# Optimization experiments

Measured on AMD Instinct MI355X. Metric: run time of the kernel, lower is better.

## Reference

```python
import jax, jax.numpy as jnp
import numpy as np

# Graph layout: B equal-sized graphs, contiguous node ids.
B, NG, EG = 64, 2000, 64000          # graphs, nodes/graph, edges/graph
K = 1600                              # ceil(0.8 * NG) — TopKPooling ratio=0.8
N, E = B * NG, B * EG
FEAT_DIM, EMB, G1, G2, DENSE, NCLS = 10000, 64, 32, 32, 64, 10


def setup_inputs() -> dict:
    key = jax.random.key(0)
    ks = jax.random.split(key, 12)
    x = jax.random.randint(ks[0], (N, 1), 0, FEAT_DIM)
    # random edges within each graph, then offset by graph base node id
    e = jax.random.randint(ks[1], (2, B, EG), 0, NG) + (jnp.arange(B) * NG)[None, :, None]
    edge_index = e.reshape(2, E)
    batch = jnp.repeat(jnp.arange(B), NG)
    sc = 0.05
    return {
        "x": x, "edge_index": edge_index, "batch": batch,
        "emb": jax.random.normal(ks[2], (FEAT_DIM, EMB), jnp.float32) * sc,
        "W1": jax.random.normal(ks[3], (EMB, G1), jnp.float32) * sc,
        "b1": jnp.zeros((G1,), jnp.float32),
        "W2": jax.random.normal(ks[4], (G1, G2), jnp.float32) * sc,
        "b2": jnp.zeros((G2,), jnp.float32),
        "pool_w": jax.random.normal(ks[5], (G2,), jnp.float32) * sc,
        "dense_W": jax.random.normal(ks[6], (G2, DENSE), jnp.float32) * sc,
        "dense_b": jnp.zeros((DENSE,), jnp.float32),
        "out_W": jax.random.normal(ks[7], (DENSE, NCLS), jnp.float32) * sc,
        "out_b": jnp.zeros((NCLS,), jnp.float32),
    }


def gcn_layer(h, src, dst, W, b):
    """PyG GCNConv: add self-loops, symmetric D^-1/2 A D^-1/2 aggregation."""
    n = h.shape[0]
    loop = jnp.arange(n)
    s = jnp.concatenate([src, loop])
    d = jnp.concatenate([dst, loop])
    h = h @ W                                                   # [N, out]
    deg = jax.ops.segment_sum(jnp.ones_like(d, dtype=h.dtype), d, num_segments=n)
    dinv = jnp.where(deg > 0, deg ** -0.5, 0.0)
    norm = dinv[s] * dinv[d]                                    # [E+N]
    out = jax.ops.segment_sum(h[s] * norm[:, None], d, num_segments=n)
    return out + b


def reference(x, edge_index, batch, emb, W1, b1, W2, b2, pool_w,
              dense_W, dense_b, out_W, out_b):
    h = emb[x[:, 0]]                                            # [N, EMB]
    src, dst = edge_index[0], edge_index[1]
    h = jax.nn.relu(gcn_layer(h, src, dst, W1, b1))
    h = jax.nn.relu(gcn_layer(h, src, dst, W2, b2))
    # TopKPooling: score = tanh(x.w / ||w||); keep top ceil(0.8*NG) per graph,
    # scale kept features by their scores. Equal graph sizes -> static shapes.
    score = jnp.tanh(h @ pool_w / jnp.linalg.norm(pool_w))      # [N]
    sb = score.reshape(B, NG)
    hb = h.reshape(B, NG, G2)
    vals, idx = jax.lax.top_k(sb, K)                            # [B, K]
    hp = jnp.take_along_axis(hb, idx[:, :, None], axis=1) * vals[:, :, None]
    g = hp.max(axis=1)                                          # global max pool [B, G2]
    d = jax.nn.relu(g @ dense_W + dense_b)
    return d @ out_W + out_b                                    # [B, NCLS]
```

## Files before the change

### kernel.cpp

```cpp
#include <hip/hip_runtime.h>
#include <hip/hip_fp16.h>
#include <math.h>

#define NB 64
#define NGRAPH 2000
#define EGRAPH 64000
#define NN (NB*NGRAPH)
#define NE (NB*EGRAPH)
#define KSEL 1600
#define FEAT 10000
#define EMBD 64
#define G1D 32
#define G2D 32
#define DENSED 64
#define NCLSD 10
#define NCHUNK 8
#define CHUNK_E (EGRAPH/NCHUNK)
#define NQD 8
#define QNODES (NGRAPH/NQD)
#define LOUT_CAP 10000
#define AGG_PARTS 4
#define NPP (NGRAPH/AGG_PARTS)


__device__ __forceinline__ float4 ld_row8h(const char* base, unsigned byteoff)
{
    uint2 u = *(const uint2*)(base + byteoff);
    __half2 p0 = *(__half2*)&u.x;
    __half2 p1 = *(__half2*)&u.y;
    float2 f0 = __half22float2(p0);
    float2 f1 = __half22float2(p1);
    return make_float4(f0.x, f0.y, f1.x, f1.y);
}

__device__ __forceinline__ void st_row8h(__half* dst, float4 v)
{
    __half2 p0 = __floats2half2_rn(v.x, v.y);
    __half2 p1 = __floats2half2_rn(v.z, v.w);
    uint2 u;
    u.x = *(unsigned*)&p0;
    u.y = *(unsigned*)&p1;
    *(uint2*)dst = u;
}

__device__ __forceinline__ void acc8h(const char* base, unsigned off,
                                      __half2& lo, __half2& hi)
{
    uint2 u = *(const uint2*)(base + off);
    lo = __hadd2(lo, *(__half2*)&u.x);
    hi = __hadd2(hi, *(__half2*)&u.y);
}

__device__ __forceinline__ float4 h2tof4(__half2 lo, __half2 hi)
{
    float2 a = __half22float2(lo);
    float2 b = __half22float2(hi);
    return make_float4(a.x, a.y, b.x, b.y);
}

__global__ __launch_bounds__(256) void prep_kernel(const int* __restrict__ ei,
                                                   int* __restrict__ chist,
                                                   const float* __restrict__ emb,
                                                   const float* __restrict__ W1,
                                                   float* __restrict__ embW)
{
    __shared__ float shmem[2048];
    const int tid = threadIdx.x;
    if (blockIdx.x < 512) {
        int* hist = (int*)shmem;
        const int lb = blockIdx.x;
        const int xcd = lb & 7, t = lb >> 3;
        const int g = xcd * 8 + (t >> 3);
        const int q = t & 7;
        const int base_e = g * EGRAPH + q * CHUNK_E;
        const int base_n = g * NGRAPH;
        for (int v = tid; v < NGRAPH; v += 256) hist[v] = 0;
        __syncthreads();
        for (int k = tid; k < CHUNK_E; k += 256) {
            int d = ei[NE + base_e + k];
            atomicAdd(&hist[d - base_n], 1);
        }
        __syncthreads();
        int* out = chist + (size_t)(g * NCHUNK + q) * NGRAPH;
        for (int v = tid; v < NGRAPH; v += 256) out[v] = hist[v];
    } else {
        float* W1s = shmem;
        for (int i = tid; i < EMBD * G1D; i += 256) W1s[i] = W1[i];
        __syncthreads();
        int id = (blockIdx.x - 512) * 256 + tid;
        int r = id >> 5, c = id & 31;
        if (r >= FEAT) return;
        const float* er = emb + r * EMBD;
        float acc = 0.f;
        #pragma unroll 8
        for (int k = 0; k < EMBD; ++k) acc += er[k] * W1s[k * G1D + c];
        embW[r * G1D + c] = acc;
    }
}

__global__ __launch_bounds__(256) void scan_graph(const int* __restrict__ chist,
                                                  float* __restrict__ dinv,
                                                  int* __restrict__ row_start)
{
    __shared__ int hist[NGRAPH];
    __shared__ int csA[256];
    __shared__ int csB[256];
    const int b = (blockIdx.x & 7) * 8 + (blockIdx.x >> 3);
    const int tid = threadIdx.x;
    const int base_n = b * NGRAPH, base_e = b * EGRAPH;
    const int* ch = chist + (size_t)b * NCHUNK * NGRAPH;

    for (int v = tid; v < NGRAPH; v += 256) {
        int tot = 0;
        #pragma unroll
        for (int q = 0; q < NCHUNK; ++q) tot += ch[q * NGRAPH + v];
        hist[v] = tot;
        dinv[base_n + v] = rsqrtf((float)(tot + 1));
    }
    __syncthreads();
    if (tid < 250) {
        int s = 0;
        #pragma unroll
        for (int i = 0; i < 8; ++i) s += hist[tid * 8 + i];
        csA[tid] = s;
    }
    __syncthreads();
    int* sb = csA; int* db = csB;
    for (int off = 1; off < 256; off <<= 1) {
        int v = 0;
        if (tid < 250) { v = sb[tid]; if (tid >= off) v += sb[tid - off]; }
        if (tid < 250) db[tid] = v;
        __syncthreads();
        int* t = sb; sb = db; db = t;
    }
    if (tid < 250) {
        int run = (tid == 0) ? 0 : sb[tid - 1];
        #pragma unroll
        for (int i = 0; i < 8; ++i) {
            int idx = tid * 8 + i;
            int c = hist[idx];
            row_start[base_n + idx] = base_e + run;
            run += c;
        }
    }
}

__global__ __launch_bounds__(1024) void mid_kernel(const int* __restrict__ ei,
                                                   const int* __restrict__ row_start,
                                                   int* __restrict__ csr,
                                                   const int* __restrict__ x,
                                                   const float* __restrict__ embW,
                                                   const float* __restrict__ dinv,
                                                   __half* __restrict__ A)
{
    __shared__ int cur[QNODES];
    __shared__ int lout[LOUT_CAP];
    const int tid = threadIdx.x;
    if (blockIdx.x < 512) {
        const int lb = blockIdx.x;
        const int xcd = lb & 7, t = lb >> 3;
        const int g = xcd * 8 + (t >> 3);
        const int qd = t & 7;
        const int base_n = g * NGRAPH;
        const int lo = qd * QNODES;
        const int base = row_start[base_n + lo];
        const int qend = (g == NB - 1 && qd == NQD - 1) ? NE
                         : row_start[base_n + lo + QNODES];
        for (int v = tid; v < QNODES; v += 1024)
            cur[v] = row_start[base_n + lo + v] - base;
        __syncthreads();
        const int4* srcp = (const int4*)(ei + g * EGRAPH);
        const int4* dstp = (const int4*)(ei + NE + g * EGRAPH);
        const int sub = base_n + lo;
        for (int k = tid; k < EGRAPH / 4; k += 1024) {
            int4 d4 = dstp[k];
            int4 s4 = srcp[k];
            int d, pos, sl;
            d = d4.x - sub;
            if ((unsigned)d < (unsigned)QNODES) {
                pos = atomicAdd(&cur[d], 1);
                sl = s4.x - base_n;
                if (pos < LOUT_CAP) lout[pos] = (sl << 6) + (sl << 3);
            }
            d = d4.y - sub;
            if ((unsigned)d < (unsigned)QNODES) {
                pos = atomicAdd(&cur[d], 1);
                sl = s4.y - base_n;
                if (pos < LOUT_CAP) lout[pos] = (sl << 6) + (sl << 3);
            }
            d = d4.z - sub;
            if ((unsigned)d < (unsigned)QNODES) {
                pos = atomicAdd(&cur[d], 1);
                sl = s4.z - base_n;
                if (pos < LOUT_CAP) lout[pos] = (sl << 6) + (sl << 3);
            }
            d = d4.w - sub;
            if ((unsigned)d < (unsigned)QNODES) {
                pos = atomicAdd(&cur[d], 1);
                sl = s4.w - base_n;
                if (pos < LOUT_CAP) lout[pos] = (sl << 6) + (sl << 3);
            }
        }
        __syncthreads();
        int size = qend - base;
        if (size > LOUT_CAP) size = LOUT_CAP;
        for (int i = tid; i < size; i += 1024)
            csr[base + i] = lout[i];
    } else {
        int id = (blockIdx.x - 512) * 1024 + tid;
        int v = id >> 3, r = id & 7;
        int xv = x[v];
        float dv = dinv[v];
        float4 e = ((const float4*)(embW + (size_t)xv * G1D))[r];
        e.x *= dv; e.y *= dv; e.z *= dv; e.w *= dv;
        st_row8h(A + (size_t)v * G1D + r * 4, e);
    }
}


__global__ __launch_bounds__(1024) void agg1_kernel(const __half* __restrict__ Ain,
                                                    const float* __restrict__ dinv,
                                                    const int* __restrict__ row_start,
                                                    const int* __restrict__ csr,
                                                    const float* __restrict__ b1,
                                                    const float* __restrict__ W2,
                                                    __half* __restrict__ Bout)
{
    __shared__ uint2 table2[NGRAPH * 9];
    __shared__ float hsh[32][G2D];
    const int lb = blockIdx.x;
    const int xcd = lb & 7, t = lb >> 3;
    const int b = xcd * 8 + (t >> 2);
    const int part = t & 3;
    const int tid = threadIdx.x;
    const int base_n = b * NGRAPH;

    {
        const uint2* src = (const uint2*)(Ain + (size_t)base_n * G1D);
        for (int i = tid; i < NGRAPH * 8; i += 1024)
            table2[(i >> 3) * 9 + (i & 7)] = src[i];
    }
    __syncthreads();

    const char* Lbase = (const char*)table2;
    const int hw = tid >> 5;
    const int hl = tid & 31;
    const int slot = hl >> 3;
    const int r = hl & 7;
    const int roff = r << 3;
    const float4 bias4 = ((const float4*)b1)[r];

    float w2c[G1D];
    #pragma unroll
    for (int k = 0; k < G1D; ++k) w2c[k] = W2[k * G2D + hl];

    const __half2 z2 = __float2half2_rn(0.f);

    const int vloc0 = part * NPP + hw * 16;
    const int vend = part * NPP + NPP;
    int v = base_n + vloc0;
    int rs = row_start[v];
    int re = (v == NN - 1) ? NE : row_start[v + 1];
    int s0 = csr[rs + slot];
    int s1 = csr[rs + slot + 4];
    int s2 = csr[rs + slot + 8];
    int s3 = csr[rs + slot + 12];

    for (int i = 0; i < 16; ++i) {
        int vloc = vloc0 + i;
        if (vloc >= vend) break;
        int re_next = (v + 1 >= NN - 1) ? NE : row_start[v + 2];
        int n0 = csr[re + slot];
        int n1 = csr[re + slot + 4];
        int n2 = csr[re + slot + 8];
        int n3 = csr[re + slot + 12];

        int me = rs + ((re - rs) & ~15);
        __half2 l0 = z2, h0 = z2, l1 = z2, h1 = z2;
        __half2 l2 = z2, h2 = z2, l3 = z2, h3 = z2;
        if (slot == 0)
            acc8h(Lbase, (unsigned)((vloc << 6) + (vloc << 3) + roff), l0, h0);
        int j = rs + slot;
        while (j < me) {
            int jn = j + 16;
            int t0 = csr[jn];
            int t1 = csr[jn + 4];
            int t2 = csr[jn + 8];
            int t3 = csr[jn + 12];
            acc8h(Lbase, (unsigned)(s0 + roff), l0, h0);
            acc8h(Lbase, (unsigned)(s1 + roff), l1, h1);
            acc8h(Lbase, (unsigned)(s2 + roff), l2, h2);
            acc8h(Lbase, (unsigned)(s3 + roff), l3, h3);
            j = jn; s0 = t0; s1 = t1; s2 = t2; s3 = t3;
        }
        {
            int jt = me + slot;
            if (jt < re)      acc8h(Lbase, (unsigned)(s0 + roff), l0, h0);
            if (jt + 4 < re)  acc8h(Lbase, (unsigned)(s1 + roff), l1, h1);
            if (jt + 8 < re)  acc8h(Lbase, (unsigned)(s2 + roff), l2, h2);
            if (jt + 12 < re) acc8h(Lbase, (unsigned)(s3 + roff), l3, h3);
        }
        float4 f0 = h2tof4(l0, h0);
        float4 f1 = h2tof4(l1, h1);
        float4 f2 = h2tof4(l2, h2);
        float4 f3 = h2tof4(l3, h3);
        float4 acc;
        acc.x = (f0.x + f1.x) + (f2.x + f3.x);
        acc.y = (f0.y + f1.y) + (f2.y + f3.y);
        acc.z = (f0.z + f1.z) + (f2.z + f3.z);
        acc.w = (f0.w + f1.w) + (f2.w + f3.w);
        #pragma unroll
        for (int off = 8; off <= 16; off <<= 1) {
            acc.x += __shfl_xor(acc.x, off, 32);
            acc.y += __shfl_xor(acc.y, off, 32);
            acc.z += __shfl_xor(acc.z, off, 32);
            acc.w += __shfl_xor(acc.w, off, 32);
        }
        float dv = dinv[v];
        if (slot == 0) {
            float4 h4;
            h4.x = fmaxf(dv * acc.x + bias4.x, 0.f);
            h4.y = fmaxf(dv * acc.y + bias4.y, 0.f);
            h4.z = fmaxf(dv * acc.z + bias4.z, 0.f);
            h4.w = fmaxf(dv * acc.w + bias4.w, 0.f);
            ((float4*)&hsh[hw][0])[r] = h4;
        }
        float o0 = 0.f, o1 = 0.f, o2 = 0.f, o3 = 0.f;
        const float4* hrow = (const float4*)&hsh[hw][0];
        #pragma unroll
        for (int q = 0; q < 8; ++q) {
            float4 hh = hrow[q];
            o0 += hh.x * w2c[4 * q + 0];
            o1 += hh.y * w2c[4 * q + 1];
            o2 += hh.z * w2c[4 * q + 2];
            o3 += hh.w * w2c[4 * q + 3];
        }
        Bout[(size_t)v * G2D + hl] = __float2half(dv * ((o0 + o1) + (o2 + o3)));
        v = v + 1;
        rs = re; re = re_next; s0 = n0; s1 = n1; s2 = n2; s3 = n3;
    }
}

__global__ __launch_bounds__(1024) void agg2_kernel(const __half* __restrict__ Bin,
                                                    const float* __restrict__ dinv,
                                                    const int* __restrict__ row_start,
                                                    const int* __restrict__ csr,
                                                    const float* __restrict__ b2,
                                                    const float* __restrict__ pool_w,
                                                    __half* __restrict__ h2out,
                                                    float* __restrict__ scores)
{
    __shared__ uint2 table2[NGRAPH * 9];
    const int lb = blockIdx.x;
    const int xcd = lb & 7, t = lb >> 3;
    const int b = xcd * 8 + (t >> 2);
    const int part = t & 3;
    const int tid = threadIdx.x;
    const int base_n = b * NGRAPH;

    {
        const uint2* src = (const uint2*)(Bin + (size_t)base_n * G1D);
        for (int i = tid; i < NGRAPH * 8; i += 1024)
            table2[(i >> 3) * 9 + (i & 7)] = src[i];
    }
    __syncthreads();

    const char* Lbase = (const char*)table2;
    const int hw = tid >> 5;
    const int hl = tid & 31;
    const int slot = hl >> 3;
    const int r = hl & 7;
    const int roff = r << 3;
    const float4 bias4 = ((const float4*)b2)[r];
    const float4 pw4 = ((const float4*)pool_w)[r];

    float pw = pool_w[hl];
    float nsq = pw * pw;
    #pragma unroll
    for (int off = 16; off; off >>= 1) nsq += __shfl_xor(nsq, off, 32);
    const float inv_norm = rsqrtf(nsq);

    const __half2 z2 = __float2half2_rn(0.f);

    const int vloc0 = part * NPP + hw * 16;
    const int vend = part * NPP + NPP;
    int v = base_n + vloc0;
    int rs = row_start[v];
    int re = (v == NN - 1) ? NE : row_start[v + 1];
    int s0 = csr[rs + slot];
    int s1 = csr[rs + slot + 4];
    int s2 = csr[rs + slot + 8];
    int s3 = csr[rs + slot + 12];

    for (int i = 0; i < 16; ++i) {
        int vloc = vloc0 + i;
        if (vloc >= vend) break;
        int re_next = (v + 1 >= NN - 1) ? NE : row_start[v + 2];
        int n0 = csr[re + slot];
        int n1 = csr[re + slot + 4];
        int n2 = csr[re + slot + 8];
        int n3 = csr[re + slot + 12];

        int me = rs + ((re - rs) & ~15);
        __half2 l0 = z2, h0 = z2, l1 = z2, h1 = z2;
        __half2 l2 = z2, h2 = z2, l3 = z2, h3 = z2;
        if (slot == 0)
            acc8h(Lbase, (unsigned)((vloc << 6) + (vloc << 3) + roff), l0, h0);
        int j = rs + slot;
        while (j < me) {
            int jn = j + 16;
            int t0 = csr[jn];
            int t1 = csr[jn + 4];
            int t2 = csr[jn + 8];
            int t3 = csr[jn + 12];
            acc8h(Lbase, (unsigned)(s0 + roff), l0, h0);
            acc8h(Lbase, (unsigned)(s1 + roff), l1, h1);
            acc8h(Lbase, (unsigned)(s2 + roff), l2, h2);
            acc8h(Lbase, (unsigned)(s3 + roff), l3, h3);
            j = jn; s0 = t0; s1 = t1; s2 = t2; s3 = t3;
        }
        {
            int jt = me + slot;
            if (jt < re)      acc8h(Lbase, (unsigned)(s0 + roff), l0, h0);
            if (jt + 4 < re)  acc8h(Lbase, (unsigned)(s1 + roff), l1, h1);
            if (jt + 8 < re)  acc8h(Lbase, (unsigned)(s2 + roff), l2, h2);
            if (jt + 12 < re) acc8h(Lbase, (unsigned)(s3 + roff), l3, h3);
        }
        float4 f0 = h2tof4(l0, h0);
        float4 f1 = h2tof4(l1, h1);
        float4 f2 = h2tof4(l2, h2);
        float4 f3 = h2tof4(l3, h3);
        float4 acc;
        acc.x = (f0.x + f1.x) + (f2.x + f3.x);
        acc.y = (f0.y + f1.y) + (f2.y + f3.y);
        acc.z = (f0.z + f1.z) + (f2.z + f3.z);
        acc.w = (f0.w + f1.w) + (f2.w + f3.w);
        #pragma unroll
        for (int off = 8; off <= 16; off <<= 1) {
            acc.x += __shfl_xor(acc.x, off, 32);
            acc.y += __shfl_xor(acc.y, off, 32);
            acc.z += __shfl_xor(acc.z, off, 32);
            acc.w += __shfl_xor(acc.w, off, 32);
        }
        float dv = dinv[v];
        float4 h4;
        h4.x = fmaxf(dv * acc.x + bias4.x, 0.f);
        h4.y = fmaxf(dv * acc.y + bias4.y, 0.f);
        h4.z = fmaxf(dv * acc.z + bias4.z, 0.f);
        h4.w = fmaxf(dv * acc.w + bias4.w, 0.f);
        if (slot == 0)
            st_row8h(h2out + (size_t)v * G2D + r * 4, h4);
        float tt = h4.x * pw4.x + h4.y * pw4.y + h4.z * pw4.z + h4.w * pw4.w;
        tt += __shfl_xor(tt, 1, 32);
        tt += __shfl_xor(tt, 2, 32);
        tt += __shfl_xor(tt, 4, 32);
        if (hl == 0) scores[v] = tanhf(tt * inv_norm);
        v = v + 1;
        rs = re; re = re_next; s0 = n0; s1 = n1; s2 = n2; s3 = n3;
    }
}

__global__ __launch_bounds__(1024) void topk_pool_mlp(const __half* __restrict__ h2,
                                                      const float* __restrict__ scores,
                                                      const float* __restrict__ dense_W,
                                                      const float* __restrict__ dense_b,
                                                      const float* __restrict__ out_W,
                                                      const float* __restrict__ out_b,
                                                      float* __restrict__ out)
{
    __shared__ unsigned keys[NGRAPH];
    __shared__ float    sval[NGRAPH];
    __shared__ unsigned char inc[NGRAPH];
    __shared__ int  hist[256];
    __shared__ int  csA[256];
    __shared__ int  csB[256];
    __shared__ int  sel[2];
    __shared__ int  redc[16];
    __shared__ float redf[128][32];
    __shared__ float redp[8][32];
    __shared__ float gvec[32];
    __shared__ float dvec[DENSED];
    const int b = (blockIdx.x & 7) * 8 + (blockIdx.x >> 3);
    const int tid = threadIdx.x;
    const int base_n = b * NGRAPH;

    for (int v = tid; v < NGRAPH; v += 1024) {
        float f = scores[base_n + v];
        sval[v] = f;
        unsigned u = __float_as_uint(f);
        keys[v] = (u & 0x80000000u) ? ~u : (u | 0x80000000u);
    }
    __syncthreads();

    unsigned T = 0;
    int need = KSEL;
    #pragma unroll
    for (int pass = 0; pass < 4; ++pass) {
        const int s = 24 - pass * 8;
        const unsigned hi_mask = (pass == 0) ? 0u : (0xFFFFFFFFu << (s + 8));
        if (tid < 256) hist[tid] = 0;
        __syncthreads();
        for (int v = tid; v < NGRAPH; v += 1024) {
            unsigned k = keys[v];
            if ((k & hi_mask) == (T & hi_mask))
                atomicAdd(&hist[(k >> s) & 255], 1);
        }
        __syncthreads();
        if (tid < 256) csA[tid] = hist[255 - tid];
        __syncthreads();
        int* sb = csA; int* db = csB;
        for (int off = 1; off < 256; off <<= 1) {
            int val = 0;
            if (tid < 256) {
                val = sb[tid];
                if (tid >= off) val += sb[tid - off];
                db[tid] = val;
            }
            __syncthreads();
            int* t = sb; sb = db; db = t;
        }
        if (tid < 256) {
            const int d = tid;
            int suf_d = sb[255 - d];
            int suf_d1 = (d == 255) ? 0 : sb[254 - d];
            if (suf_d >= need && suf_d1 < need) {
                sel[0] = d;
                sel[1] = suf_d1;
            }
        }
        __syncthreads();
        T |= ((unsigned)sel[0]) << s;
        need -= sel[1];
        __syncthreads();
    }

    const int wid = tid >> 6, ln = tid & 63;
    int cg = 0, ce = 0;
    for (int v = tid; v < NGRAPH; v += 1024) {
        cg += (keys[v] > T) ? 1 : 0;
        ce += (keys[v] == T) ? 1 : 0;
    }
    int packed = (cg << 16) | ce;
    #pragma unroll
    for (int off = 32; off; off >>= 1) packed += __shfl_down(packed, off, 64);
    if (ln == 0) redc[wid] = packed;
    __syncthreads();
    int tot = 0;
    #pragma unroll
    for (int w = 0; w < 16; ++w) tot += redc[w];
    int m_gt = tot >> 16, m_eq = tot & 0xffff;
    int needed = KSEL - m_gt;
    float fT = (T & 0x80000000u) ? __uint_as_float(T & 0x7fffffffu)
                                 : __uint_as_float(~T);
    if (m_eq == needed || fT == 0.0f) {
        for (int v = tid; v < NGRAPH; v += 1024) inc[v] = (keys[v] >= T) ? 1 : 0;
    } else {
        if (tid == 0) {
            int take = 0;
            for (int v = 0; v < NGRAPH; ++v) {
                unsigned k = keys[v];
                if (k > T) inc[v] = 1;
                else if (k == T && take < needed) { inc[v] = 1; ++take; }
                else inc[v] = 0;
            }
        }
    }
    __syncthreads();

    {
        const int rowslot = tid >> 3;
        const int c4 = tid & 7;
        float4 m4 = make_float4(-INFINITY, -INFINITY, -INFINITY, -INFINITY);
        const char* h2base = (const char*)h2;
        for (int v = rowslot; v < NGRAPH; v += 128) {
            float4 hrow = ld_row8h(h2base,
                                   (unsigned)((base_n + v) * (G2D * 2) + c4 * 8));
            float sv = inc[v] ? sval[v] : 0.f;
            float big = inc[v] ? 0.f : -INFINITY;
            m4.x = fmaxf(m4.x, sv * hrow.x + big);
            m4.y = fmaxf(m4.y, sv * hrow.y + big);
            m4.z = fmaxf(m4.z, sv * hrow.z + big);
            m4.w = fmaxf(m4.w, sv * hrow.w + big);
        }
        redf[rowslot][c4 * 4 + 0] = m4.x;
        redf[rowslot][c4 * 4 + 1] = m4.y;
        redf[rowslot][c4 * 4 + 2] = m4.z;
        redf[rowslot][c4 * 4 + 3] = m4.w;
    }
    __syncthreads();
    if (tid < 256) {
        const int col = tid & 31, part = tid >> 5;
        float g = redf[part * 16][col];
        #pragma unroll
        for (int rr = 1; rr < 16; ++rr) g = fmaxf(g, redf[part * 16 + rr][col]);
        redp[part][col] = g;
    }
    __syncthreads();
    if (tid < 32) {
        float g = redp[0][tid];
        #pragma unroll
        for (int p = 1; p < 8; ++p) g = fmaxf(g, redp[p][tid]);
        gvec[tid] = g;
    }
    __syncthreads();
    if (tid < DENSED) {
        float t = dense_b[tid];
        #pragma unroll
        for (int k = 0; k < G2D; ++k) t += gvec[k] * dense_W[k * DENSED + tid];
        dvec[tid] = fmaxf(t, 0.f);
    }
    __syncthreads();
    if (tid < NCLSD) {
        float o = out_b[tid];
        #pragma unroll
        for (int j = 0; j < DENSED; ++j) o += dvec[j] * out_W[j * NCLSD + tid];
        out[b * NCLSD + tid] = o;
    }
}

extern "C" void kernel_launch(void* const* d_in, const int* in_sizes, int n_in,
                              void* d_out, int out_size, void* d_ws, size_t ws_size,
                              hipStream_t stream)
{
    (void)in_sizes; (void)n_in; (void)out_size; (void)ws_size;
    const int*   x       = (const int*)  d_in[0];
    const int*   edge    = (const int*)  d_in[1];
    const float* emb     = (const float*)d_in[3];
    const float* W1      = (const float*)d_in[4];
    const float* b1      = (const float*)d_in[5];
    const float* W2      = (const float*)d_in[6];
    const float* b2      = (const float*)d_in[7];
    const float* pool_w  = (const float*)d_in[8];
    const float* dense_W = (const float*)d_in[9];
    const float* dense_b = (const float*)d_in[10];
    const float* out_W   = (const float*)d_in[11];
    const float* out_b   = (const float*)d_in[12];
    float* outp = (float*)d_out;

    char* ws = (char*)d_ws;
    float*  embW      = (float*)ws;
    __half* Ah        = (__half*)(ws + 1280000);
    __half* Bh        = (__half*)(ws + 1280000 + 8192000);
    float*  dinv      = (float*)(ws + 1280000 + 2*8192000);
    int*    row_start = (int*)((char*)dinv + (size_t)NN*4);
    int*    csr       = (int*)((char*)row_start + (size_t)NN*4);
    float*  scores    = (float*)((char*)csr + (size_t)(NE+16)*4);

    int* chist = (int*)Bh;

    prep_kernel<<<512 + (FEAT * G1D) / 256, 256, 0, stream>>>(edge, chist, emb, W1, embW);
    scan_graph<<<NB, 256, 0, stream>>>(chist, dinv, row_start);
    mid_kernel<<<512 + (NN * 8) / 1024, 1024, 0, stream>>>(edge, row_start, csr,
                                                           x, embW, dinv, Ah);
    agg1_kernel<<<NB * AGG_PARTS, 1024, 0, stream>>>(Ah, dinv, row_start, csr, b1, W2, Bh);
    agg2_kernel<<<NB * AGG_PARTS, 1024, 0, stream>>>(Bh, dinv, row_start, csr, b2, pool_w, Ah, scores);
    topk_pool_mlp<<<NB, 1024, 0, stream>>>(Ah, scores, dense_W, dense_b, out_W, out_b, outp);
}
```

Measured before the change: 213.8 us.

## Build CSR from per-chunk offsets instead of dst-range edge rescans

The scan kernel now turns the per-chunk destination histograms into exclusive per-chunk write offsets. The CSR fill kernel then gives each block one edge chunk and scatters directly into global CSR through shared-memory atomic cursors. Before, each block read all edges of its graph and kept only one destination range, so every graph's edges were read eight times. The cost is scattered global writes in place of coalesced stores from a shared buffer, though the LOUT_CAP truncation risk goes away.

```diff
diff --git a/kernel.cpp b/kernel.cpp
--- a/kernel.cpp
+++ b/kernel.cpp
@@ -16,9 +16,6 @@
 #define NCLSD 10
 #define NCHUNK 8
 #define CHUNK_E (EGRAPH/NCHUNK)
-#define NQD 8
-#define QNODES (NGRAPH/NQD)
-#define LOUT_CAP 10000
 #define AGG_PARTS 4
 #define NPP (NGRAPH/AGG_PARTS)
 
@@ -98,7 +95,7 @@
     }
 }
 
-__global__ __launch_bounds__(256) void scan_graph(const int* __restrict__ chist,
+__global__ __launch_bounds__(256) void scan_graph(int* __restrict__ chist,
                                                   float* __restrict__ dinv,
                                                   int* __restrict__ row_start)
 {
@@ -108,7 +105,7 @@
     const int b = (blockIdx.x & 7) * 8 + (blockIdx.x >> 3);
     const int tid = threadIdx.x;
     const int base_n = b * NGRAPH, base_e = b * EGRAPH;
-    const int* ch = chist + (size_t)b * NCHUNK * NGRAPH;
+    int* ch = chist + (size_t)b * NCHUNK * NGRAPH;
 
     for (int v = tid; v < NGRAPH; v += 256) {
         int tot = 0;
@@ -140,72 +137,57 @@
             int idx = tid * 8 + i;
             int c = hist[idx];
             row_start[base_n + idx] = base_e + run;
+            hist[idx] = base_e + run;
             run += c;
         }
     }
+    __syncthreads();
+    for (int v = tid; v < NGRAPH; v += 256) {
+        int run = hist[v];
+        #pragma unroll
+        for (int q = 0; q < NCHUNK; ++q) {
+            int c = ch[q * NGRAPH + v];
+            ch[q * NGRAPH + v] = run;
+            run += c;
+        }
+    }
 }
 
 __global__ __launch_bounds__(1024) void mid_kernel(const int* __restrict__ ei,
-                                                   const int* __restrict__ row_start,
+                                                   const int* __restrict__ cbase,
                                                    int* __restrict__ csr,
                                                    const int* __restrict__ x,
                                                    const float* __restrict__ embW,
                                                    const float* __restrict__ dinv,
                                                    __half* __restrict__ A)
 {
-    __shared__ int cur[QNODES];
-    __shared__ int lout[LOUT_CAP];
+    __shared__ int cur[NGRAPH];
     const int tid = threadIdx.x;
     if (blockIdx.x < 512) {
         const int lb = blockIdx.x;
         const int xcd = lb & 7, t = lb >> 3;
         const int g = xcd * 8 + (t >> 3);
-        const int qd = t & 7;
+        const int q = t & 7;
         const int base_n = g * NGRAPH;
-        const int lo = qd * QNODES;
-        const int base = row_start[base_n + lo];
-        const int qend = (g == NB - 1 && qd == NQD - 1) ? NE
-                         : row_start[base_n + lo + QNODES];
-        for (int v = tid; v < QNODES; v += 1024)
-            cur[v] = row_start[base_n + lo + v] - base;
-        __syncthreads();
-        const int4* srcp = (const int4*)(ei + g * EGRAPH);
-        const int4* dstp = (const int4*)(ei + NE + g * EGRAPH);
-        const int sub = base_n + lo;
-        for (int k = tid; k < EGRAPH / 4; k += 1024) {
+        const int* cb = cbase + (size_t)(g * NCHUNK + q) * NGRAPH;
+        for (int v = tid; v < NGRAPH; v += 1024) cur[v] = cb[v];
+        __syncthreads();
+        const int base_e4 = (g * EGRAPH + q * CHUNK_E) >> 2;
+        const int4* srcp = (const int4*)ei + base_e4;
+        const int4* dstp = (const int4*)(ei + NE) + base_e4;
+        for (int k = tid; k < CHUNK_E / 4; k += 1024) {
             int4 d4 = dstp[k];
             int4 s4 = srcp[k];
-            int d, pos, sl;
-            d = d4.x - sub;
-            if ((unsigned)d < (unsigned)QNODES) {
-                pos = atomicAdd(&cur[d], 1);
-                sl = s4.x - base_n;
-                if (pos < LOUT_CAP) lout[pos] = (sl << 6) + (sl << 3);
-            }
-            d = d4.y - sub;
-            if ((unsigned)d < (unsigned)QNODES) {
-                pos = atomicAdd(&cur[d], 1);
-                sl = s4.y - base_n;
-                if (pos < LOUT_CAP) lout[pos] = (sl << 6) + (sl << 3);
-            }
-            d = d4.z - sub;
-            if ((unsigned)d < (unsigned)QNODES) {
-                pos = atomicAdd(&cur[d], 1);
-                sl = s4.z - base_n;
-                if (pos < LOUT_CAP) lout[pos] = (sl << 6) + (sl << 3);
-            }
-            d = d4.w - sub;
-            if ((unsigned)d < (unsigned)QNODES) {
-                pos = atomicAdd(&cur[d], 1);
-                sl = s4.w - base_n;
-                if (pos < LOUT_CAP) lout[pos] = (sl << 6) + (sl << 3);
-            }
-        }
-        __syncthreads();
-        int size = qend - base;
-        if (size > LOUT_CAP) size = LOUT_CAP;
-        for (int i = tid; i < size; i += 1024)
-            csr[base + i] = lout[i];
+            int pos, sl;
+            pos = atomicAdd(&cur[d4.x - base_n], 1);
+            sl = s4.x - base_n; csr[pos] = (sl << 6) + (sl << 3);
+            pos = atomicAdd(&cur[d4.y - base_n], 1);
+            sl = s4.y - base_n; csr[pos] = (sl << 6) + (sl << 3);
+            pos = atomicAdd(&cur[d4.z - base_n], 1);
+            sl = s4.z - base_n; csr[pos] = (sl << 6) + (sl << 3);
+            pos = atomicAdd(&cur[d4.w - base_n], 1);
+            sl = s4.w - base_n; csr[pos] = (sl << 6) + (sl << 3);
+        }
     } else {
         int id = (blockIdx.x - 512) * 1024 + tid;
         int v = id >> 3, r = id & 7;
@@ -650,7 +632,7 @@
 
     prep_kernel<<<512 + (FEAT * G1D) / 256, 256, 0, stream>>>(edge, chist, emb, W1, embW);
     scan_graph<<<NB, 256, 0, stream>>>(chist, dinv, row_start);
-    mid_kernel<<<512 + (NN * 8) / 1024, 1024, 0, stream>>>(edge, row_start, csr,
+    mid_kernel<<<512 + (NN * 8) / 1024, 1024, 0, stream>>>(edge, chist, csr,
                                                            x, embW, dinv, Ah);
     agg1_kernel<<<NB * AGG_PARTS, 1024, 0, stream>>>(Ah, dinv, row_start, csr, b1, W2, Bh);
     agg2_kernel<<<NB * AGG_PARTS, 1024, 0, stream>>>(Bh, dinv, row_start, csr, b2, pool_w, Ah, scores);
```

New measurement: 216.3 us. About the same (+1.1%).
